# Kernel optimization log

Measured on AMD Instinct MI355X. Metric: run time of the kernel, lower is better.

The kernel has to match this reference:

```python
import jax, jax.numpy as jnp
import numpy as np

B, NT, D = 256, 301, 96
NSEG = 50


def setup_inputs() -> dict:
    key = jax.random.key(0)
    inp = jax.random.normal(key, (B, NT, D), dtype=jnp.float32)
    return {"inp": inp, "n_segments": NSEG}


def _logsig_depth2(segs):
    # segs: (B, S, L, D) -- per-segment sub-paths (piecewise linear)
    x0 = segs[:, :, :1, :]
    dx = segs[:, :, 1:, :] - segs[:, :, :-1, :]          # increments (B,S,L-1,D)
    xprev = segs[:, :, :-1, :] - x0                      # X(t-) - X(0)
    lvl1 = segs[:, :, -1, :] - segs[:, :, 0, :]          # level-1 logsig (B,S,D)
    # Level-2 signature S_ij = sum_t X_i(t-) dX_j + 0.5 sum_t dX_i dX_j;
    # log-signature level 2 is the antisymmetric part (Levy area), so the
    # symmetric 0.5 dx (x) dx term cancels and we only need M - M^T.
    M = jnp.einsum('bsti,bstj->bsij', xprev, dx)         # (B,S,D,D)
    A = 0.5 * (M - jnp.swapaxes(M, -1, -2))
    iu, ju = np.triu_indices(segs.shape[-1], k=1)
    # words/Lyndon basis at depth 2: coefficients A_ij for i<j, lexicographic
    return jnp.concatenate([lvl1, A[:, :, iu, ju]], axis=-1)


def reference(inp, n_segments):
    # n_segments is a static Python int -> segment index map built at trace time,
    # replicating: t_vec = [round(x) for x in linspace(1, nT, n_segments+1)],
    # segment i = inp[:, t_vec[i]-1 : t_vec[i+1], :]
    nT = inp.shape[1]
    t_vec = [int(round(x)) for x in np.linspace(1, nT, n_segments + 1)]
    idx = np.stack([np.arange(t_vec[i] - 1, t_vec[i + 1]) for i in range(n_segments)])  # (S, L)
    segs = inp[:, idx, :]                                # (B, S, L, D)
    return _logsig_depth2(segs)
```

## Files before the change

### kernel.cpp

```cpp
#include <hip/hip_runtime.h>

#define BB 256
#define NT 301
#define DD 96
#define NSEG 50
#define SEGROWS 7
#define NTRI (DD * (DD - 1) / 2)
#define OUTD (DD + NTRI)

__global__ __launch_bounds__(256)
void logsig_kernel(const float* __restrict__ inp, float* __restrict__ out) {
    const int bs = blockIdx.x;
    const int b  = bs / NSEG;
    const int s  = bs % NSEG;

    __shared__ float seg[SEGROWS * DD];

    const float* src = inp + ((size_t)b * NT + (size_t)6 * s) * DD;
    for (int idx = threadIdx.x; idx < SEGROWS * DD; idx += 256)
        seg[idx] = src[idx];
    __syncthreads();

    float* o = out + (size_t)bs * OUTD;

    if (threadIdx.x < DD)
        o[threadIdx.x] = seg[6 * DD + threadIdx.x] - seg[threadIdx.x];

    const int ty = threadIdx.x >> 4;
    const int tx = threadIdx.x & 15;

    for (int ti = 0; ti < 6; ++ti) {
        const int i = 16 * ti + ty;
        float si[SEGROWS];
        #pragma unroll
        for (int t = 0; t < SEGROWS; ++t) si[t] = seg[t * DD + i];

        for (int tj = ti; tj < 6; ++tj) {
            const int j = 16 * tj + tx;
            if (j > i) {
                float sj[SEGROWS];
                #pragma unroll
                for (int t = 0; t < SEGROWS; ++t) sj[t] = seg[t * DD + j];

                float acc = 0.f;
                #pragma unroll
                for (int t = 1; t < 6; ++t) {
                    const float xpi = si[t] - si[0];
                    const float dxj = sj[t + 1] - sj[t];
                    const float xpj = sj[t] - sj[0];
                    const float dxi = si[t + 1] - si[t];
                    acc += xpi * dxj - xpj * dxi;
                }
                const int tri = i * (2 * DD - 1 - i) / 2 + (j - i - 1);
                o[DD + tri] = 0.5f * acc;
            }
        }
    }
}

extern "C" void kernel_launch(void* const* d_in, const int* in_sizes, int n_in,
                              void* d_out, int out_size, void* d_ws, size_t ws_size,
                              hipStream_t stream) {
    const float* inp = (const float*)d_in[0];
    float* out = (float*)d_out;
    logsig_kernel<<<BB * NSEG, 256, 0, stream>>>(inp, out);
}
```

Baseline: 289.3 us.

## Transpose segment to column-major smem and simplify Levy area algebra with register-cached rows

Stores the segment in shared memory column-major with padding so each coordinate's 7 samples load as two float4 reads. The Levy-area sum is rewritten algebraically into a telescoped form using adjacent-sample cross products, with the 0.5 factor prefolded into cached row values. Row data for all six i-tiles is held in registers, and the loop is inverted over j-tiles and fully unrolled. This cuts shared-memory loads and arithmetic per output, at the cost of higher register pressure under the 4-block occupancy hint.

```diff
diff --git a/kernel.cpp b/kernel.cpp
--- a/kernel.cpp
+++ b/kernel.cpp
@@ -1,58 +1,71 @@
 #include <hip/hip_runtime.h>
 
 #define BB 256
-#define NT 301
+#define NT_ 301
 #define DD 96
 #define NSEG 50
 #define SEGROWS 7
 #define NTRI (DD * (DD - 1) / 2)
 #define OUTD (DD + NTRI)
+#define CS 12
 
-__global__ __launch_bounds__(256)
+
+__global__ __launch_bounds__(256, 4)
 void logsig_kernel(const float* __restrict__ inp, float* __restrict__ out) {
     const int bs = blockIdx.x;
     const int b  = bs / NSEG;
-    const int s  = bs % NSEG;
+    const int s  = bs - b * NSEG;
 
-    __shared__ float seg[SEGROWS * DD];
+    __shared__ float colp[DD * CS];
 
-    const float* src = inp + ((size_t)b * NT + (size_t)6 * s) * DD;
-    for (int idx = threadIdx.x; idx < SEGROWS * DD; idx += 256)
-        seg[idx] = src[idx];
+    const float* __restrict__ src = inp + ((size_t)b * NT_ + (size_t)(6 * s)) * DD;
+    for (int idx = threadIdx.x; idx < SEGROWS * DD; idx += 256) {
+        const int r = idx / DD;
+        const int c = idx - r * DD;
+        colp[c * CS + r] = src[idx];
+    }
     __syncthreads();
-
-    float* o = out + (size_t)bs * OUTD;
-
-    if (threadIdx.x < DD)
-        o[threadIdx.x] = seg[6 * DD + threadIdx.x] - seg[threadIdx.x];
 
     const int ty = threadIdx.x >> 4;
     const int tx = threadIdx.x & 15;
 
+    float rs[6][8];
+    int rowoff[6];
+    #pragma unroll
     for (int ti = 0; ti < 6; ++ti) {
         const int i = 16 * ti + ty;
-        float si[SEGROWS];
+        const float4 lo = *reinterpret_cast<const float4*>(&colp[i * CS]);
+        const float4 hi = *reinterpret_cast<const float4*>(&colp[i * CS + 4]);
+        rs[ti][0] = 0.5f * lo.x; rs[ti][1] = 0.5f * lo.y;
+        rs[ti][2] = 0.5f * lo.z; rs[ti][3] = 0.5f * lo.w;
+        rs[ti][4] = 0.5f * hi.x; rs[ti][5] = 0.5f * hi.y;
+        rs[ti][6] = 0.5f * hi.z;
+        rs[ti][7] = rs[ti][6] - rs[ti][1];
+        rowoff[ti] = DD + (i * (2 * DD - 1 - i)) / 2 - i - 1;
+    }
+
+    float* __restrict__ o = out + (size_t)bs * OUTD;
+
+    #pragma unroll
+    for (int tj = 0; tj < 6; ++tj) {
+        const int j = 16 * tj + tx;
+        const float4 lo = *reinterpret_cast<const float4*>(&colp[j * CS]);
+        const float4 hi = *reinterpret_cast<const float4*>(&colp[j * CS + 4]);
+        const float c0 = lo.x, c1 = lo.y, c2 = lo.z, c3 = lo.w;
+        const float c4 = hi.x, c5 = hi.y, c6 = hi.z;
+        const float uj = c6 - c1;
+        if (ty == 0)
+            o[j] = c6 - c0;
         #pragma unroll
-        for (int t = 0; t < SEGROWS; ++t) si[t] = seg[t * DD + i];
-
-        for (int tj = ti; tj < 6; ++tj) {
-            const int j = 16 * tj + tx;
-            if (j > i) {
-                float sj[SEGROWS];
-                #pragma unroll
-                for (int t = 0; t < SEGROWS; ++t) sj[t] = seg[t * DD + j];
-
-                float acc = 0.f;
-                #pragma unroll
-                for (int t = 1; t < 6; ++t) {
-                    const float xpi = si[t] - si[0];
-                    const float dxj = sj[t + 1] - sj[t];
-                    const float xpj = sj[t] - sj[0];
-                    const float dxi = si[t + 1] - si[t];
-                    acc += xpi * dxj - xpj * dxi;
-                }
-                const int tri = i * (2 * DD - 1 - i) / 2 + (j - i - 1);
-                o[DD + tri] = 0.5f * acc;
+        for (int ti = 0; ti <= tj; ++ti) {
+            if (ti < tj || tx > ty) {
+                float acc  = rs[ti][7] * c0 - rs[ti][0] * uj;
+                acc += rs[ti][1] * c2 - rs[ti][2] * c1;
+                acc += rs[ti][2] * c3 - rs[ti][3] * c2;
+                acc += rs[ti][3] * c4 - rs[ti][4] * c3;
+                acc += rs[ti][4] * c5 - rs[ti][5] * c4;
+                acc += rs[ti][5] * c6 - rs[ti][6] * c5;
+                o[rowoff[ti] + j] = acc;
             }
         }
     }
```

After: 307.2 us. 1.06x slower.
